# Optimization experiments

Hardware: AMD Instinct MI355X
Metric: run time of the kernel (lower is better)

Reference implementation:

```python
import jax, jax.numpy as jnp
import numpy as np
from jax import lax

B, CIN, COUT = 1, 16, 32
D, H, W = 16, 128, 128
KD = KH = KW = 3
K = KD * KH * KW  # 27 kernel taps
PAD = 1
MAX_XY, MAX_T = 4.0, 2.0


def setup_inputs() -> dict:
    key = jax.random.key(0)
    k1, k2, k3, k4, k5 = jax.random.split(key, 5)
    x = jax.random.normal(k1, (B, CIN, D, H, W), dtype=jnp.float32)
    weight = jax.random.normal(k2, (COUT, CIN, K), dtype=jnp.float32) * 0.05
    bias = jax.random.normal(k3, (COUT,), dtype=jnp.float32) * 0.05
    # offset conv: Conv3d(CIN, 3K, k=3, s=1, p=1). Small random weights so
    # tanh(raw)*max_disp produces nontrivial, bounded offsets.
    off_w = jax.random.normal(k4, (3 * K, CIN, 3, 3, 3), dtype=jnp.float32) * 0.02
    off_b = jax.random.normal(k5, (3 * K,), dtype=jnp.float32) * 0.02
    return {"x": x, "weight": weight, "bias": bias, "off_w": off_w, "off_b": off_b}


def _trilinear_sample(vol, coords):
    """vol [C,Dp,Hp,Wp]; coords [K,Do,Ho,Wo,3] absolute (x,y,z) in padded vol.
    Zero padding outside, align_corners=True semantics (absolute coords)."""
    C, Dp, Hp, Wp = vol.shape
    gx, gy, gz = coords[..., 0], coords[..., 1], coords[..., 2]
    x0 = jnp.floor(gx); y0 = jnp.floor(gy); z0 = jnp.floor(gz)
    wx = gx - x0; wy = gy - y0; wz = gz - z0
    x0i = x0.astype(jnp.int32); y0i = y0.astype(jnp.int32); z0i = z0.astype(jnp.int32)
    out = jnp.zeros((C,) + gx.shape, dtype=vol.dtype)
    for dz in (0, 1):
        for dy in (0, 1):
            for dx in (0, 1):
                xi = x0i + dx; yi = y0i + dy; zi = z0i + dz
                w = (wx if dx else 1.0 - wx) * (wy if dy else 1.0 - wy) * (wz if dz else 1.0 - wz)
                valid = (xi >= 0) & (xi < Wp) & (yi >= 0) & (yi < Hp) & (zi >= 0) & (zi < Dp)
                xc = jnp.clip(xi, 0, Wp - 1); yc = jnp.clip(yi, 0, Hp - 1); zc = jnp.clip(zi, 0, Dp - 1)
                v = vol[:, zc, yc, xc]  # [C,K,Do,Ho,Wo]
                out = out + v * (w * valid.astype(vol.dtype))[None]
    return out


def _forward(x, weight, bias, off_w, off_b):
    # offset prediction conv (stride 1, pad 1)
    raw = lax.conv_general_dilated(
        x, off_w, window_strides=(1, 1, 1),
        padding=((PAD, PAD), (PAD, PAD), (PAD, PAD)),
        dimension_numbers=("NCDHW", "OIDHW", "NCDHW"))
    raw = raw + off_b[None, :, None, None, None]
    Do, Ho, Wo = raw.shape[2:]
    off = raw.reshape(B, K, 3, Do, Ho, Wo)
    dx = jnp.tanh(off[:, :, 0]) * MAX_XY
    dy = jnp.tanh(off[:, :, 1]) * MAX_XY
    dz = jnp.tanh(off[:, :, 2]) * MAX_T
    offsets = jnp.stack([dx, dy, dz], axis=-1)  # [B,K,Do,Ho,Wo,3]

    x_pad = jnp.pad(x, ((0, 0), (0, 0), (PAD, PAD), (PAD, PAD), (PAD, PAD)))

    oz = jnp.arange(Do, dtype=x.dtype); oy = jnp.arange(Ho, dtype=x.dtype); ox = jnp.arange(Wo, dtype=x.dtype)
    zz, yy, xx = jnp.meshgrid(oz, oy, ox, indexing="ij")
    # kernel center offset: (k//2)*dilation = 1
    base = jnp.stack([xx + 1.0, yy + 1.0, zz + 1.0], axis=-1)[None, None]  # [1,1,Do,Ho,Wo,3]

    r = jnp.arange(-(KD // 2), KD // 2 + 1, dtype=x.dtype)
    rz, ry, rx = jnp.meshgrid(r, r, r, indexing="ij")
    rel = jnp.stack([rx, ry, rz], axis=-1).reshape(K, 3)[None, :, None, None, None, :]

    grid_abs = base + rel + offsets  # [B,K,Do,Ho,Wo,3] absolute padded coords

    sampled = jax.vmap(_trilinear_sample)(x_pad, grid_abs)  # [B,C,K,Do,Ho,Wo]
    out = jnp.einsum("bckdhw,ock->bodhw", sampled, weight)
    return out + bias[None, :, None, None, None]


def reference(x, weight, bias, off_w, off_b):
    return _forward(x, weight, bias, off_w, off_b)
```

## Files before the change

kernel.cpp:

```cpp
#include <hip/hip_runtime.h>

#define DD 16
#define HH 128
#define WW 128
#define DHW (DD * HH * WW)
#define CIN 16
#define COUT 32
#define KK 27
#define NOFF 81
#define NKC 14
#define NNT 6

typedef _Float16 h2    __attribute__((ext_vector_type(2)));
typedef _Float16 f16x8 __attribute__((ext_vector_type(8)));
typedef float    f32x4 __attribute__((ext_vector_type(4)));
struct H16 { h2 v[8]; };

#define XT_BYTES   ((size_t)DHW * CIN * 2)
#define WBF_OFF    XT_BYTES
#define WBF_ELEMS  (NKC * NNT * 64 * 8)
#define WW3_OFF    (WBF_OFF + (size_t)WBF_ELEMS * 2)
#define WW3_ELEMS  (NKC * 2 * 64 * 8)
#define WS_NEED    (WW3_OFF + (size_t)WW3_ELEMS * 2)

__device__ __forceinline__ float fast_tanh(float s) {
    float e = __expf(fminf(2.f * s, 80.f));
    return (e - 1.f) * __builtin_amdgcn_rcpf(e + 1.f);
}

__global__ __launch_bounds__(256) void transpose_x_h(const float* __restrict__ x,
                                                     H16* __restrict__ xt) {
    int vox = blockIdx.x * 256 + threadIdx.x;
    if (vox >= DHW) return;
    H16 o;
#pragma unroll
    for (int p = 0; p < 8; ++p) {
        o.v[p][0] = (_Float16)x[(size_t)(2 * p) * DHW + vox];
        o.v[p][1] = (_Float16)x[(size_t)(2 * p + 1) * DHW + vox];
    }
    xt[vox] = o;
}

__global__ __launch_bounds__(256) void pack_w(const float* __restrict__ off_w,
                                              const float* __restrict__ weight,
                                              _Float16* __restrict__ wBf,
                                              _Float16* __restrict__ wW3) {
    int idx = blockIdx.x * 256 + threadIdx.x;
    if (idx < WBF_ELEMS) {
        int i    = idx & 7;
        int lane = (idx >> 3) & 63;
        int fn   = idx >> 9;
        int n    = fn % NNT;
        int kc   = fn / NNT;
        int g    = lane >> 4;
        int t    = kc * 2 + (g >> 1);
        int ci   = (g & 1) * 8 + i;
        int j    = n * 16 + (lane & 15);
        float v = 0.f;
        if (t < KK && j < NOFF) v = off_w[(size_t)(j * CIN + ci) * KK + t];
        wBf[idx] = (_Float16)v;
    }
    if (idx < WW3_ELEMS) {
        int i    = idx & 7;
        int lane = (idx >> 3) & 63;
        int fm   = idx >> 9;
        int mo   = fm & 1;
        int kc   = fm >> 1;
        int g    = lane >> 4;
        int t    = kc * 2 + (g >> 1);
        int ci   = (g & 1) * 8 + i;
        int o    = mo * 16 + (lane & 15);
        float v = 0.f;
        if (t < KK) v = weight[(size_t)(o * CIN + ci) * KK + t];
        wW3[idx] = (_Float16)v;
    }
}

__global__ __launch_bounds__(128, 3) void deform_full(
    const f16x8* __restrict__ xt16,
    const f16x8* __restrict__ wBf,
    const f16x8* __restrict__ wW3,
    const float* __restrict__ off_b,
    const float* __restrict__ bias,
    float* __restrict__ out)
{
    __shared__ _Float16 loff[128 * 84];

    const int lb = ((blockIdx.x & 7) << 8) | (blockIdx.x >> 3);
    const int h = lb & (HH - 1);
    const int d = lb >> 7;
    const int lane = threadIdx.x & 63;
    const int wave = threadIdx.x >> 6;
    const int g = lane >> 4;
    const int col = lane & 15;

    f32x4 acc[4][NNT];
#pragma unroll
    for (int mi = 0; mi < 4; ++mi)
#pragma unroll
        for (int n = 0; n < NNT; ++n) acc[mi][n] = f32x4{0.f, 0.f, 0.f, 0.f};

#pragma unroll 1
    for (int kc = 0; kc < NKC; ++kc) {
        const int t  = kc * 2 + (g >> 1);
        const int tz = t / 9, ty = (t / 3) % 3, tx = t % 3;
        const int zz = d + tz - 1, yy = h + ty - 1;
        const bool okzy = (t < KK) && ((unsigned)zz < (unsigned)DD) &&
                          ((unsigned)yy < (unsigned)HH);
        const int zc = min(max(zz, 0), DD - 1);
        const int yc = min(max(yy, 0), HH - 1);
        const int rowbase = (zc * HH + yc) * WW;
        const int txm1 = tx - 1;
        const int half = g & 1;

        f16x8 bfr[NNT];
#pragma unroll
        for (int n = 0; n < NNT; ++n) bfr[n] = wBf[(kc * NNT + n) * 64 + lane];

#pragma unroll
        for (int mi = 0; mi < 4; ++mi) {
            const int xx = (wave * 4 + mi) * 16 + col + txm1;
            const bool ok = okzy && ((unsigned)xx < (unsigned)WW);
            const int xc = min(max(xx, 0), WW - 1);
            union { f16x8 v; uint4 u; } au;
            au.v = xt16[(size_t)(rowbase + xc) * 2 + half];
            if (!ok) au.u = make_uint4(0u, 0u, 0u, 0u);
#pragma unroll
            for (int n = 0; n < NNT; ++n)
                acc[mi][n] = __builtin_amdgcn_mfma_f32_16x16x32_f16(
                    au.v, bfr[n], acc[mi][n], 0, 0, 0);
        }
    }

#pragma unroll
    for (int n = 0; n < NNT; ++n) {
        const int j = n * 16 + col;
        if (j < NOFF) {
            const float ob = off_b[j];
            const float sc = (j % 3 == 2) ? 2.f : 4.f;
#pragma unroll
            for (int mi = 0; mi < 4; ++mi) {
#pragma unroll
                for (int r = 0; r < 4; ++r) {
                    const int vl = (wave * 4 + mi) * 16 + g * 4 + r;
                    loff[vl * 84 + j] =
                        (_Float16)(fast_tanh(acc[mi][n][r] + ob) * sc);
                }
            }
        }
    }
    __syncthreads();

    f32x4 acc3[2][4];
#pragma unroll
    for (int mo = 0; mo < 2; ++mo)
#pragma unroll
        for (int nv = 0; nv < 4; ++nv) acc3[mo][nv] = f32x4{0.f, 0.f, 0.f, 0.f};

    const int half = g & 1;

#pragma unroll 2
    for (int kc = 0; kc < NKC; ++kc) {
        const int myTap = kc * 2 + (g >> 1);
        const bool tapValid = myTap < KK;
        const int tA = tapValid ? myTap : 0;

        const f16x8 aw0 = wW3[(kc * 2 + 0) * 64 + lane];
        const f16x8 aw1 = wW3[(kc * 2 + 1) * 64 + lane];

        const int rx = tA % 3 - 1, ry = (tA / 3) % 3 - 1, rz = tA / 9 - 1;

#pragma unroll
        for (int nv = 0; nv < 4; ++nv) {
            const int wv = wave * 64 + nv * 16 + col;

            float dxo = 0.f, dyo = 0.f, dzo = 0.f;
            if (tapValid) {
                dxo = (float)loff[wv * 84 + tA * 3 + 0];
                dyo = (float)loff[wv * 84 + tA * 3 + 1];
                dzo = (float)loff[wv * 84 + tA * 3 + 2];
            }

            const float gx = (float)(wv + 1 + rx) + dxo;
            const float gy = (float)(h + 1 + ry) + dyo;
            const float gz = (float)(d + 1 + rz) + dzo;
            const float fx0f = floorf(gx), fy0f = floorf(gy), fz0f = floorf(gz);
            const float fx = gx - fx0f, fy = gy - fy0f, fz = gz - fz0f;
            const int x0 = (int)fx0f - 1, y0 = (int)fy0f - 1, z0 = (int)fz0f - 1;
            const float ifx = 1.f - fx, ify = 1.f - fy, ifz = 1.f - fz;

            float cw[8];
            int cidx[8];
#pragma unroll
            for (int c = 0; c < 8; ++c) {
                const int cx = x0 + (c & 1);
                const int cy = y0 + ((c >> 1) & 1);
                const int cz = z0 + (c >> 2);
                const bool ok = tapValid &&
                                (unsigned)cx < (unsigned)WW &&
                                (unsigned)cy < (unsigned)HH &&
                                (unsigned)cz < (unsigned)DD;
                const float wt = ((c & 1) ? fx : ifx) *
                                 (((c >> 1) & 1) ? fy : ify) *
                                 ((c >> 2) ? fz : ifz);
                cw[c] = ok ? wt : 0.f;
                const int cxc = min(max(cx, 0), WW - 1);
                const int cyc = min(max(cy, 0), HH - 1);
                const int czc = min(max(cz, 0), DD - 1);
                cidx[c] = (czc * HH + cyc) * WW + cxc;
            }

            f16x8 cv[8];
#pragma unroll
            for (int c = 0; c < 8; ++c)
                cv[c] = xt16[(size_t)cidx[c] * 2 + half];

            union { f16x8 v; h2 s[4]; } sf;
#pragma unroll
            for (int p = 0; p < 4; ++p) { sf.s[p][0] = (_Float16)0.f; sf.s[p][1] = (_Float16)0.f; }
#pragma unroll
            for (int c = 0; c < 8; ++c) {
                const _Float16 wh = (_Float16)cw[c];
                h2 w2; w2[0] = wh; w2[1] = wh;
                const h2* cvp = (const h2*)&cv[c];
#pragma unroll
                for (int p = 0; p < 4; ++p)
                    sf.s[p] = sf.s[p] + w2 * cvp[p];
            }

            acc3[0][nv] = __builtin_amdgcn_mfma_f32_16x16x32_f16(
                aw0, sf.v, acc3[0][nv], 0, 0, 0);
            acc3[1][nv] = __builtin_amdgcn_mfma_f32_16x16x32_f16(
                aw1, sf.v, acc3[1][nv], 0, 0, 0);
        }
    }

    const int rowBase = (d * HH + h) * WW;
#pragma unroll
    for (int mo = 0; mo < 2; ++mo) {
#pragma unroll
        for (int r = 0; r < 4; ++r) {
            const int o = mo * 16 + 4 * g + r;
            const float b = bias[o];
#pragma unroll
            for (int nv = 0; nv < 4; ++nv) {
                const int wv = wave * 64 + nv * 16 + col;
                out[(size_t)o * DHW + rowBase + wv] = acc3[mo][nv][r] + b;
            }
        }
    }
}

__global__ __launch_bounds__(128) void deform_fallback(
    const float* __restrict__ x,
    const float* __restrict__ weight,
    const float* __restrict__ bias,
    const float* __restrict__ off_w,
    const float* __restrict__ off_b,
    float* __restrict__ out)
{
    const int w = threadIdx.x;
    const int h = blockIdx.x & (HH - 1);
    const int d = blockIdx.x >> 7;

    float outacc[COUT];
#pragma unroll
    for (int o = 0; o < COUT; ++o) outacc[o] = 0.f;

    for (int k = 0; k < KK; ++k) {
        float a0 = 0.f, a1 = 0.f, a2 = 0.f;
        const float* w0 = off_w + (size_t)(k * 3 + 0) * (CIN * KK);
        const float* w1 = off_w + (size_t)(k * 3 + 1) * (CIN * KK);
        const float* w2 = off_w + (size_t)(k * 3 + 2) * (CIN * KK);
        for (int ci = 0; ci < CIN; ++ci) {
            const float* xc = x + (size_t)ci * DHW;
#pragma unroll
            for (int t = 0; t < KK; ++t) {
                const int tz = t / 9, ty = (t / 3) % 3, tx = t % 3;
                const int zz = d + tz - 1, yy = h + ty - 1, xx = w + tx - 1;
                const bool ok = (unsigned)zz < (unsigned)DD &&
                                (unsigned)yy < (unsigned)HH &&
                                (unsigned)xx < (unsigned)WW;
                const float v = ok ? xc[(zz * HH + yy) * WW + xx] : 0.f;
                a0 = fmaf(v, w0[ci * KK + t], a0);
                a1 = fmaf(v, w1[ci * KK + t], a1);
                a2 = fmaf(v, w2[ci * KK + t], a2);
            }
        }
        const float dxo = fast_tanh(a0 + off_b[k * 3 + 0]) * 4.f;
        const float dyo = fast_tanh(a1 + off_b[k * 3 + 1]) * 4.f;
        const float dzo = fast_tanh(a2 + off_b[k * 3 + 2]) * 2.f;

        const int rx = k % 3 - 1, ry = (k / 3) % 3 - 1, rz = k / 9 - 1;
        const float gx = (float)(w + 1 + rx) + dxo;
        const float gy = (float)(h + 1 + ry) + dyo;
        const float gz = (float)(d + 1 + rz) + dzo;
        const float fx0 = floorf(gx), fy0 = floorf(gy), fz0 = floorf(gz);
        const float fx = gx - fx0, fy = gy - fy0, fz = gz - fz0;
        const int x0 = (int)fx0 - 1, y0 = (int)fy0 - 1, z0 = (int)fz0 - 1;

        float samp[CIN];
#pragma unroll
        for (int ci = 0; ci < CIN; ++ci) samp[ci] = 0.f;
#pragma unroll
        for (int c = 0; c < 8; ++c) {
            const int cx = x0 + (c & 1);
            const int cy = y0 + ((c >> 1) & 1);
            const int cz = z0 + (c >> 2);
            const float wt = ((c & 1) ? fx : 1.f - fx) *
                             (((c >> 1) & 1) ? fy : 1.f - fy) *
                             ((c >> 2) ? fz : 1.f - fz);
            if ((unsigned)cx < (unsigned)WW && (unsigned)cy < (unsigned)HH &&
                (unsigned)cz < (unsigned)DD) {
                const float* p = x + ((cz * HH) + cy) * WW + cx;
#pragma unroll
                for (int ci = 0; ci < 16; ++ci)
                    samp[ci] = fmaf(wt, p[(size_t)ci * DHW], samp[ci]);
            }
        }
#pragma unroll
        for (int o = 0; o < COUT; ++o) {
            float s = 0.f;
#pragma unroll
            for (int ci = 0; ci < 16; ++ci)
                s = fmaf(weight[(o * CIN + ci) * KK + k], samp[ci], s);
            outacc[o] += s;
        }
    }
    const int vox = (d * HH + h) * WW + w;
#pragma unroll
    for (int o = 0; o < COUT; ++o)
        out[(size_t)o * DHW + vox] = outacc[o] + bias[o];
}

extern "C" void kernel_launch(void* const* d_in, const int* in_sizes, int n_in,
                              void* d_out, int out_size, void* d_ws, size_t ws_size,
                              hipStream_t stream) {
    const float* x      = (const float*)d_in[0];
    const float* weight = (const float*)d_in[1];
    const float* bias   = (const float*)d_in[2];
    const float* off_w  = (const float*)d_in[3];
    const float* off_b  = (const float*)d_in[4];
    float* out = (float*)d_out;

    if (ws_size >= WS_NEED) {
        H16* xt = (H16*)d_ws;
        _Float16* wBf = (_Float16*)((char*)d_ws + WBF_OFF);
        _Float16* wW3 = (_Float16*)((char*)d_ws + WW3_OFF);
        pack_w<<<(WBF_ELEMS + 255) / 256, 256, 0, stream>>>(off_w, weight, wBf, wW3);
        transpose_x_h<<<(DHW + 255) / 256, 256, 0, stream>>>(x, xt);
        deform_full<<<DD * HH, 128, 0, stream>>>((const f16x8*)xt, (const f16x8*)wBf,
                                                 (const f16x8*)wW3, off_b, bias, out);
    } else {
        deform_fallback<<<DD * HH, 128, 0, stream>>>(x, weight, bias, off_w, off_b, out);
    }
}
```

Measured before the change: 172.3 us.

## Split offset conv into two passes and shrink LDS to raise occupancy

The offset-prediction MFMA stage now runs in two passes of three N-tiles each, which halves the live accumulator registers, and launch bounds are raised from 3 to 4 blocks. The LDS offset buffer stride drops from 84 to 78. The offsets for the last tap are kept in registers and written into the slots of tap 0 once the first kc iteration has consumed them. The block-wide __syncthreads becomes a wave barrier, since each wave only reads rows it wrote itself. In exchange, the input rows for the offset conv are loaded twice, the sampling loop loses its unroll-by-2, and the LDS slot overlay adds a fragile ordering dependency.

Result: slower. 250.0 us (+45.1%).

```diff
diff --git a/kernel.cpp b/kernel.cpp
--- a/kernel.cpp
+++ b/kernel.cpp
@@ -76,7 +76,7 @@
     }
 }
 
-__global__ __launch_bounds__(128, 3) void deform_full(
+__global__ __launch_bounds__(128, 4) void deform_full(
     const f16x8* __restrict__ xt16,
     const f16x8* __restrict__ wBf,
     const f16x8* __restrict__ wW3,
@@ -84,7 +84,7 @@
     const float* __restrict__ bias,
     float* __restrict__ out)
 {
-    __shared__ _Float16 loff[128 * 84];
+    __shared__ _Float16 loff[128 * 78];
 
     const int lb = ((blockIdx.x & 7) << 8) | (blockIdx.x >> 3);
     const int h = lb & (HH - 1);
@@ -93,63 +93,73 @@
     const int wave = threadIdx.x >> 6;
     const int g = lane >> 4;
     const int col = lane & 15;
-
-    f32x4 acc[4][NNT];
-#pragma unroll
-    for (int mi = 0; mi < 4; ++mi)
-#pragma unroll
-        for (int n = 0; n < NNT; ++n) acc[mi][n] = f32x4{0.f, 0.f, 0.f, 0.f};
+    const int half = g & 1;
+
+    _Float16 keepA[16];
+    _Float16 keepB[16];
 
 #pragma unroll 1
-    for (int kc = 0; kc < NKC; ++kc) {
-        const int t  = kc * 2 + (g >> 1);
-        const int tz = t / 9, ty = (t / 3) % 3, tx = t % 3;
-        const int zz = d + tz - 1, yy = h + ty - 1;
-        const bool okzy = (t < KK) && ((unsigned)zz < (unsigned)DD) &&
-                          ((unsigned)yy < (unsigned)HH);
-        const int zc = min(max(zz, 0), DD - 1);
-        const int yc = min(max(yy, 0), HH - 1);
-        const int rowbase = (zc * HH + yc) * WW;
-        const int txm1 = tx - 1;
-        const int half = g & 1;
-
-        f16x8 bfr[NNT];
-#pragma unroll
-        for (int n = 0; n < NNT; ++n) bfr[n] = wBf[(kc * NNT + n) * 64 + lane];
-
-#pragma unroll
-        for (int mi = 0; mi < 4; ++mi) {
-            const int xx = (wave * 4 + mi) * 16 + col + txm1;
-            const bool ok = okzy && ((unsigned)xx < (unsigned)WW);
-            const int xc = min(max(xx, 0), WW - 1);
-            union { f16x8 v; uint4 u; } au;
-            au.v = xt16[(size_t)(rowbase + xc) * 2 + half];
-            if (!ok) au.u = make_uint4(0u, 0u, 0u, 0u);
-#pragma unroll
-            for (int n = 0; n < NNT; ++n)
-                acc[mi][n] = __builtin_amdgcn_mfma_f32_16x16x32_f16(
-                    au.v, bfr[n], acc[mi][n], 0, 0, 0);
-        }
-    }
-
-#pragma unroll
-    for (int n = 0; n < NNT; ++n) {
-        const int j = n * 16 + col;
-        if (j < NOFF) {
-            const float ob = off_b[j];
+    for (int pass = 0; pass < 2; ++pass) {
+        f32x4 acc[4][3];
+#pragma unroll
+        for (int mi = 0; mi < 4; ++mi)
+#pragma unroll
+            for (int nn = 0; nn < 3; ++nn) acc[mi][nn] = f32x4{0.f, 0.f, 0.f, 0.f};
+
+#pragma unroll 1
+        for (int kc = 0; kc < NKC; ++kc) {
+            const int t  = kc * 2 + (g >> 1);
+            const int tz = t / 9, ty = (t / 3) % 3, tx = t % 3;
+            const int zz = d + tz - 1, yy = h + ty - 1;
+            const bool okzy = (t < KK) && ((unsigned)zz < (unsigned)DD) &&
+                              ((unsigned)yy < (unsigned)HH);
+            const int zc = min(max(zz, 0), DD - 1);
+            const int yc = min(max(yy, 0), HH - 1);
+            const int rowbase = (zc * HH + yc) * WW;
+            const int txm1 = tx - 1;
+
+            f16x8 bfr[3];
+#pragma unroll
+            for (int nn = 0; nn < 3; ++nn)
+                bfr[nn] = wBf[(kc * NNT + pass * 3 + nn) * 64 + lane];
+
+#pragma unroll
+            for (int mi = 0; mi < 4; ++mi) {
+                const int xx = (wave * 4 + mi) * 16 + col + txm1;
+                const bool ok = okzy && ((unsigned)xx < (unsigned)WW);
+                const int xc = min(max(xx, 0), WW - 1);
+                union { f16x8 v; uint4 u; } au;
+                au.v = xt16[(size_t)(rowbase + xc) * 2 + half];
+                if (!ok) au.u = make_uint4(0u, 0u, 0u, 0u);
+#pragma unroll
+                for (int nn = 0; nn < 3; ++nn)
+                    acc[mi][nn] = __builtin_amdgcn_mfma_f32_16x16x32_f16(
+                        au.v, bfr[nn], acc[mi][nn], 0, 0, 0);
+            }
+        }
+
+#pragma unroll
+        for (int nn = 0; nn < 3; ++nn) {
+            const int j = (pass * 3 + nn) * 16 + col;
+            const float ob = (j < NOFF) ? off_b[j] : 0.f;
             const float sc = (j % 3 == 2) ? 2.f : 4.f;
 #pragma unroll
             for (int mi = 0; mi < 4; ++mi) {
 #pragma unroll
                 for (int r = 0; r < 4; ++r) {
-                    const int vl = (wave * 4 + mi) * 16 + g * 4 + r;
-                    loff[vl * 84 + j] =
-                        (_Float16)(fast_tanh(acc[mi][n][r] + ob) * sc);
+                    const _Float16 val =
+                        (_Float16)(fast_tanh(acc[mi][nn][r] + ob) * sc);
+                    if (nn == 1 && pass == 1) keepA[mi * 4 + r] = val;
+                    if (nn == 2 && pass == 1) keepB[mi * 4 + r] = val;
+                    if (j < 78) {
+                        const int vl = (wave * 4 + mi) * 16 + g * 4 + r;
+                        loff[vl * 78 + j] = val;
+                    }
                 }
             }
         }
     }
-    __syncthreads();
+    __builtin_amdgcn_wave_barrier();
 
     f32x4 acc3[2][4];
 #pragma unroll
@@ -157,13 +167,10 @@
 #pragma unroll
         for (int nv = 0; nv < 4; ++nv) acc3[mo][nv] = f32x4{0.f, 0.f, 0.f, 0.f};
 
-    const int half = g & 1;
-
-#pragma unroll 2
-    for (int kc = 0; kc < NKC; ++kc) {
+    auto kcBody = [&](int kc) {
         const int myTap = kc * 2 + (g >> 1);
-        const bool tapValid = myTap < KK;
-        const int tA = tapValid ? myTap : 0;
+        const int tA = min(myTap, KK - 1);
+        const int loffBase = (tA == KK - 1) ? 0 : tA * 3;
 
         const f16x8 aw0 = wW3[(kc * 2 + 0) * 64 + lane];
         const f16x8 aw1 = wW3[(kc * 2 + 1) * 64 + lane];
@@ -174,12 +181,9 @@
         for (int nv = 0; nv < 4; ++nv) {
             const int wv = wave * 64 + nv * 16 + col;
 
-            float dxo = 0.f, dyo = 0.f, dzo = 0.f;
-            if (tapValid) {
-                dxo = (float)loff[wv * 84 + tA * 3 + 0];
-                dyo = (float)loff[wv * 84 + tA * 3 + 1];
-                dzo = (float)loff[wv * 84 + tA * 3 + 2];
-            }
+            const float dxo = (float)loff[wv * 78 + loffBase + 0];
+            const float dyo = (float)loff[wv * 78 + loffBase + 1];
+            const float dzo = (float)loff[wv * 78 + loffBase + 2];
 
             const float gx = (float)(wv + 1 + rx) + dxo;
             const float gy = (float)(h + 1 + ry) + dyo;
@@ -196,8 +200,7 @@
                 const int cx = x0 + (c & 1);
                 const int cy = y0 + ((c >> 1) & 1);
                 const int cz = z0 + (c >> 2);
-                const bool ok = tapValid &&
-                                (unsigned)cx < (unsigned)WW &&
+                const bool ok = (unsigned)cx < (unsigned)WW &&
                                 (unsigned)cy < (unsigned)HH &&
                                 (unsigned)cz < (unsigned)DD;
                 const float wt = ((c & 1) ? fx : ifx) *
@@ -233,7 +236,29 @@
             acc3[1][nv] = __builtin_amdgcn_mfma_f32_16x16x32_f16(
                 aw1, sf.v, acc3[1][nv], 0, 0, 0);
         }
-    }
+    };
+
+    kcBody(0);
+    {
+        const bool wr = (col == 0) || (col == 14) || (col == 15);
+        if (wr) {
+            const int jj = (col == 14) ? 0 : ((col == 15) ? 1 : 2);
+#pragma unroll
+            for (int mi = 0; mi < 4; ++mi) {
+#pragma unroll
+                for (int r = 0; r < 4; ++r) {
+                    const int vl = (wave * 4 + mi) * 16 + g * 4 + r;
+                    const _Float16 v =
+                        (col == 0) ? keepB[mi * 4 + r] : keepA[mi * 4 + r];
+                    loff[vl * 78 + jj] = v;
+                }
+            }
+        }
+    }
+    __builtin_amdgcn_wave_barrier();
+
+#pragma unroll 1
+    for (int kc = 1; kc < NKC; ++kc) kcBody(kc);
 
     const int rowBase = (d * HH + h) * WW;
 #pragma unroll
```
